# Optimization experiments

Hardware: AMD Instinct MI355X
Metric: run time of the kernel (lower is better)

Reference implementation:

```python
import jax, jax.numpy as jnp
import numpy as np
from jax import lax

ALPHA = 5.0   # ATan surrogate alpha
TAU = 2.0     # LIF tau
HEADS = 16
SCALE = 0.25

@jax.custom_vjp
def atan_spike(x):
    return (x >= 0.0).astype(x.dtype)

def _atan_fwd(x):
    return atan_spike(x), x

def _atan_bwd(x, g):
    # spikingjelly surrogate.ATan: d/dx = alpha/2 / (1 + (pi/2*alpha*x)^2)
    return (g * (ALPHA / 2.0) / (1.0 + (jnp.pi / 2.0 * ALPHA * x) ** 2),)

atan_spike.defvjp(_atan_fwd, _atan_bwd)

def lif(x, v_th=1.0):
    # Multi-step LIF, hard reset to 0, detach_reset=True. x: [T, ...]
    def step(v, xt):
        h = v + (xt - v) / TAU
        s = atan_spike(h - v_th)
        v_new = h * (1.0 - lax.stop_gradient(s))
        return v_new, s
    _, spikes = lax.scan(step, jnp.zeros_like(x[0]), x)
    return spikes

def conv_bn(x, w, gamma, beta, mean, var, eps=1e-5):
    # 1x1 Conv1d (bias=False) + BatchNorm1d (eval stats). x: [..., C, N]
    y = jnp.einsum('oc,...cn->...on', w, x)
    scale = gamma * lax.rsqrt(var + eps)
    return y * scale[:, None] + (beta - mean * scale)[:, None]

def setup_inputs() -> dict:
    key = jax.random.key(0)
    ks = jax.random.split(key, 22)
    T, B, C, H, W = 4, 8, 256, 32, 16
    d = {}
    d['x'] = jax.random.normal(ks[0], (T, B, C, H, W), jnp.float32)
    i = 1
    for n in ['q', 'k', 'v', 'proj']:
        d[n + '_w'] = jax.random.normal(ks[i], (C, C), jnp.float32) / 16.0; i += 1
        d[n + '_gamma'] = jax.random.uniform(ks[i], (C,), jnp.float32, 0.5, 1.5); i += 1
        d[n + '_beta'] = jax.random.normal(ks[i], (C,), jnp.float32) * 0.1; i += 1
        d[n + '_mean'] = jax.random.normal(ks[i], (C,), jnp.float32) * 0.1; i += 1
        d[n + '_var'] = jax.random.uniform(ks[i], (C,), jnp.float32, 0.5, 1.5); i += 1
    return d

def reference(x, q_w, q_gamma, q_beta, q_mean, q_var,
              k_w, k_gamma, k_beta, k_mean, k_var,
              v_w, v_gamma, v_beta, v_mean, v_var,
              proj_w, proj_gamma, proj_beta, proj_mean, proj_var):
    T, B, C, H, W = x.shape
    N = H * W
    hd = C // HEADS
    xf = x.reshape(T, B, C, N)

    def branch(w, g, b, m, v):
        s = lif(conv_bn(xf, w, g, b, m, v))  # [T,B,C,N] binary spikes
        # -> [T,B,heads,N,head_dim]
        return s.transpose(0, 1, 3, 2).reshape(T, B, N, HEADS, hd).transpose(0, 1, 3, 2, 4)

    q = branch(q_w, q_gamma, q_beta, q_mean, q_var)
    k = branch(k_w, k_gamma, k_beta, k_mean, k_var)
    v = branch(v_w, v_gamma, v_beta, v_mean, v_var)

    attn = jnp.einsum('tbhnd,tbhmd->tbhnm', q, k)           # binary q@k^T
    y = jnp.einsum('tbhnm,tbhmd->tbhnd', attn, v) * SCALE   # (attn @ v) * 0.25
    y = y.transpose(0, 1, 2, 4, 3).reshape(T, B, C, N)       # transpose(3,4) then merge heads

    # attn_lif is applied on flatten(0,1): time dim = T*B (faithful to source)
    s = lif(y.reshape(T * B, C, N), v_th=0.5)
    p = conv_bn(s, proj_w, proj_gamma, proj_beta, proj_mean, proj_var)
    out = lif(p.reshape(T, B, C, W, H))  # note W,H swap, as in source
    return out
```

## Files before the change

### kernel.cpp

```cpp
#include <hip/hip_runtime.h>

#define TT 4
#define BB 8
#define CC 256
#define NN 512
#define HEADS 16
#define HD 16

#define GLL16(gp, lp) \
    __builtin_amdgcn_global_load_lds( \
        (const __attribute__((address_space(1))) void*)(gp), \
        (__attribute__((address_space(3))) void*)(lp), 16, 0, 0)

struct WPtrs  { const float* w[4]; };
struct BnPtrs { const float* g[4]; const float* b[4]; const float* m[4]; const float* v[4]; };

__global__ __launch_bounds__(256)
void prep_bn(BnPtrs p, float* __restrict__ sc, float* __restrict__ bi)
{
    int m = blockIdx.x, c = threadIdx.x;
    float rs = __fdiv_rn(1.0f, __fsqrt_rn(__fadd_rn(p.v[m][c], 1e-5f)));
    float s  = __fmul_rn(p.g[m][c], rs);
    sc[m * CC + c] = s;
    bi[m * CC + c] = __fsub_rn(p.b[m][c], __fmul_rn(p.m[m][c], s));
}

__global__ __launch_bounds__(256)
void transpose_w(WPtrs p, float* __restrict__ wt)
{
    __shared__ float t[16][17];
    const int m  = blockIdx.z;
    const float* w = p.w[m];
    const int o0 = blockIdx.y * 16, k0 = blockIdx.x * 16;
    const int tx = threadIdx.x, ty = threadIdx.y;
    t[ty][tx] = w[(size_t)(o0 + ty) * CC + k0 + tx];
    __syncthreads();
    wt[(size_t)m * CC * CC + (size_t)(k0 + ty) * CC + o0 + tx] = t[tx][ty];
}

__global__ __launch_bounds__(256)
void qkv_conv_bn_lif_pack(const float* __restrict__ x,
                          const float* __restrict__ wt,
                          const float* __restrict__ scA,
                          const float* __restrict__ biA,
                          unsigned long long* __restrict__ bits)
{
    __shared__ float Wl[2][32][128];
    __shared__ float Xl[2][32][128];
    __shared__ unsigned char Spk[128][16];

    const int tid = threadIdx.x;
    const int tx = tid & 15;
    const int ty = tid >> 4;
    const int br = blockIdx.z >> 3;
    const int b  = blockIdx.z & 7;
    const int o0 = blockIdx.y * 128;
    const int n0 = blockIdx.x * 128;

    const float* wb = wt + (size_t)br * CC * CC;
    unsigned long long* bout = bits + (size_t)br * (TT * BB * CC * 8);

    float sc[8], bi[8];
#pragma unroll
    for (int i = 0; i < 8; ++i) {
        sc[i] = scA[br * CC + o0 + ty * 8 + i];
        bi[i] = biA[br * CC + o0 + ty * 8 + i];
    }

    auto stage = [&](int s, int buf) {
        const int t  = s >> 3;
        const int k0 = (s & 7) * 32;
        const float* xb = x + (size_t)(t * BB + b) * (CC * NN);
#pragma unroll
        for (int i = 0; i < 4; ++i) {
            int idx = tid + 256 * i;
            int row = idx >> 5, cg = idx & 31;
            GLL16(&wb[(size_t)(k0 + row) * CC + o0 + cg * 4], &Wl[buf][row][cg * 4]);
        }
#pragma unroll
        for (int i = 0; i < 4; ++i) {
            int idx = tid + 256 * i;
            int row = idx >> 5, cg = idx & 31;
            GLL16(&xb[(size_t)(k0 + row) * NN + n0 + cg * 4], &Xl[buf][row][cg * 4]);
        }
    };

    float acc[8][8], vst[8][8];
#pragma unroll
    for (int i = 0; i < 8; ++i)
#pragma unroll
        for (int j = 0; j < 8; ++j) { acc[i][j] = 0.0f; vst[i][j] = 0.0f; }

    stage(0, 0);
    __syncthreads();

    int cur = 0;
    for (int s = 0; s < 32; ++s) {
        if (s < 31) stage(s + 1, cur ^ 1);

#pragma unroll 8
        for (int kk = 0; kk < 32; ++kk) {
            const float4 w0 = *reinterpret_cast<const float4*>(&Wl[cur][kk][ty * 8]);
            const float4 w1 = *reinterpret_cast<const float4*>(&Wl[cur][kk][ty * 8 + 4]);
            const float4 x0 = *reinterpret_cast<const float4*>(&Xl[cur][kk][tx * 8]);
            const float4 x1 = *reinterpret_cast<const float4*>(&Xl[cur][kk][tx * 8 + 4]);
            const float wa[8] = {w0.x, w0.y, w0.z, w0.w, w1.x, w1.y, w1.z, w1.w};
            const float xa[8] = {x0.x, x0.y, x0.z, x0.w, x1.x, x1.y, x1.z, x1.w};
#pragma unroll
            for (int i = 0; i < 8; ++i)
#pragma unroll
                for (int j = 0; j < 8; ++j)
                    acc[i][j] = __fmaf_rn(wa[i], xa[j], acc[i][j]);
        }

        if ((s & 7) == 7) {
            const int t = s >> 3;
#pragma unroll
            for (int i = 0; i < 8; ++i) {
                unsigned int byte = 0u;
#pragma unroll
                for (int j = 0; j < 8; ++j) {
                    float ybn = __fadd_rn(__fmul_rn(acc[i][j], sc[i]), bi[i]);
                    float h   = __fadd_rn(vst[i][j],
                                          __fmul_rn(__fsub_rn(ybn, vst[i][j]), 0.5f));
                    bool sp = (h >= 1.0f);
                    vst[i][j] = sp ? 0.0f : h;
                    byte |= (sp ? 1u : 0u) << j;
                    acc[i][j] = 0.0f;
                }
                Spk[ty * 8 + i][tx] = (unsigned char)byte;
            }
            __syncthreads();
            {
                int o = tid >> 1, ch = tid & 1;
                unsigned long long m =
                    *reinterpret_cast<const unsigned long long*>(&Spk[o][ch * 8]);
                bout[((size_t)(t * BB + b) * CC + o0 + o) * 8 + (blockIdx.x * 2 + ch)] = m;
            }
        }

        __syncthreads();
        cur ^= 1;
    }
}

__global__ __launch_bounds__(256)
void attn_kernel(const unsigned long long* __restrict__ bq,
                 const unsigned long long* __restrict__ bk,
                 const unsigned long long* __restrict__ bv,
                 float* __restrict__ y)
{
    const int blk = blockIdx.x;
    const int h  = blk & 15;
    const int tb = blk >> 4;
    const int tid = threadIdx.x;

    __shared__ unsigned long long kb[16][8], vb[16][8], qb[16][8];
    __shared__ float M[16][16];

    size_t base = ((size_t)tb * CC + h * HD) * 8;
    if (tid < 128) {
        int j = tid >> 3, ch = tid & 7;
        kb[j][ch] = bk[base + j * 8 + ch];
        vb[j][ch] = bv[base + j * 8 + ch];
        qb[j][ch] = bq[base + j * 8 + ch];
    }
    __syncthreads();

    {
        int j = tid >> 4, d = tid & 15;
        int cnt = 0;
#pragma unroll
        for (int ch = 0; ch < 8; ++ch)
            cnt += __popcll(kb[j][ch] & vb[d][ch]);
        M[j][d] = (float)cnt;
    }
    __syncthreads();

    size_t ybase = ((size_t)tb * CC + h * HD) * (size_t)NN;
#pragma unroll
    for (int r = 0; r < 2; ++r) {
        int n = tid + 256 * r;
        int ch = n >> 6, sh = n & 63;
        float acc[16];
#pragma unroll
        for (int d = 0; d < 16; ++d) acc[d] = 0.0f;
#pragma unroll
        for (int j = 0; j < 16; ++j) {
            float bit = (float)((qb[j][ch] >> sh) & 1ULL);
#pragma unroll
            for (int d = 0; d < 16; ++d)
                acc[d] = __fmaf_rn(bit, M[j][d], acc[d]);
        }
#pragma unroll
        for (int d = 0; d < 16; ++d)
            y[ybase + (size_t)d * NN + n] = __fmul_rn(acc[d], 0.25f);
    }
}

__global__ __launch_bounds__(256)
void attn_lif(float* __restrict__ y)
{
    const int e = blockIdx.x * 256 + threadIdx.x;
    float xs[32];
#pragma unroll
    for (int tb = 0; tb < 32; ++tb)
        xs[tb] = y[(size_t)tb * (CC * NN) + e];
    float v = 0.0f;
#pragma unroll
    for (int tb = 0; tb < 32; ++tb) {
        float h = __fadd_rn(v, __fmul_rn(__fsub_rn(xs[tb], v), 0.5f));
        bool sp = (h >= 0.5f);
        y[(size_t)tb * (CC * NN) + e] = sp ? 1.0f : 0.0f;
        v = sp ? 0.0f : h;
    }
}

__global__ __launch_bounds__(256)
void proj_gemm_bn(const float* __restrict__ X,
                  const float* __restrict__ wtp,
                  const float* __restrict__ scP,
                  const float* __restrict__ biP,
                  float* __restrict__ Y)
{
    __shared__ float Wl[2][32][128];
    __shared__ float Xl[2][32][128];

    const int tid = threadIdx.x;
    const int tx = tid & 15;
    const int ty = tid >> 4;
    const int tb = blockIdx.z;
    const int o0 = blockIdx.y * 128;
    const int n0 = blockIdx.x * 128;

    const float* xb = X + (size_t)tb * (CC * NN);

    float sc[8], bi[8];
#pragma unroll
    for (int i = 0; i < 8; ++i) {
        sc[i] = scP[o0 + ty * 8 + i];
        bi[i] = biP[o0 + ty * 8 + i];
    }

    auto stage = [&](int s, int buf) {
        const int k0 = s * 32;
#pragma unroll
        for (int i = 0; i < 4; ++i) {
            int idx = tid + 256 * i;
            int row = idx >> 5, cg = idx & 31;
            GLL16(&wtp[(size_t)(k0 + row) * CC + o0 + cg * 4], &Wl[buf][row][cg * 4]);
        }
#pragma unroll
        for (int i = 0; i < 4; ++i) {
            int idx = tid + 256 * i;
            int row = idx >> 5, cg = idx & 31;
            GLL16(&xb[(size_t)(k0 + row) * NN + n0 + cg * 4], &Xl[buf][row][cg * 4]);
        }
    };

    float acc[8][8];
#pragma unroll
    for (int i = 0; i < 8; ++i)
#pragma unroll
        for (int j = 0; j < 8; ++j) acc[i][j] = 0.0f;

    stage(0, 0);
    __syncthreads();

    int cur = 0;
    for (int s = 0; s < 8; ++s) {
        if (s < 7) stage(s + 1, cur ^ 1);

#pragma unroll 8
        for (int kk = 0; kk < 32; ++kk) {
            const float4 w0 = *reinterpret_cast<const float4*>(&Wl[cur][kk][ty * 8]);
            const float4 w1 = *reinterpret_cast<const float4*>(&Wl[cur][kk][ty * 8 + 4]);
            const float4 x0 = *reinterpret_cast<const float4*>(&Xl[cur][kk][tx * 8]);
            const float4 x1 = *reinterpret_cast<const float4*>(&Xl[cur][kk][tx * 8 + 4]);
            const float wa[8] = {w0.x, w0.y, w0.z, w0.w, w1.x, w1.y, w1.z, w1.w};
            const float xa[8] = {x0.x, x0.y, x0.z, x0.w, x1.x, x1.y, x1.z, x1.w};
#pragma unroll
            for (int i = 0; i < 8; ++i)
#pragma unroll
                for (int j = 0; j < 8; ++j)
                    acc[i][j] = __fmaf_rn(wa[i], xa[j], acc[i][j]);
        }

        __syncthreads();
        cur ^= 1;
    }

    float* Yp = Y + (size_t)tb * (CC * NN);
#pragma unroll
    for (int i = 0; i < 8; ++i) {
        float r[8];
#pragma unroll
        for (int j = 0; j < 8; ++j)
            r[j] = __fadd_rn(__fmul_rn(acc[i][j], sc[i]), bi[i]);
        float4 r0 = make_float4(r[0], r[1], r[2], r[3]);
        float4 r1 = make_float4(r[4], r[5], r[6], r[7]);
        float* dst = &Yp[(size_t)(o0 + ty * 8 + i) * NN + n0 + tx * 8];
        *reinterpret_cast<float4*>(dst) = r0;
        *reinterpret_cast<float4*>(dst + 4) = r1;
    }
}

__global__ __launch_bounds__(256)
void final_lif(const float* __restrict__ Yp, float* __restrict__ out)
{
    const size_t stride = (size_t)BB * CC * NN;
    const int i4 = blockIdx.x * 256 + threadIdx.x;
    float4 v = make_float4(0.f, 0.f, 0.f, 0.f);
#pragma unroll
    for (int t = 0; t < 4; ++t) {
        float4 xv = *reinterpret_cast<const float4*>(&Yp[t * stride + (size_t)i4 * 4]);
        float4 o4;
        float h;
        h = __fadd_rn(v.x, __fmul_rn(__fsub_rn(xv.x, v.x), 0.5f));
        o4.x = (h >= 1.0f) ? 1.0f : 0.0f; v.x = (h >= 1.0f) ? 0.0f : h;
        h = __fadd_rn(v.y, __fmul_rn(__fsub_rn(xv.y, v.y), 0.5f));
        o4.y = (h >= 1.0f) ? 1.0f : 0.0f; v.y = (h >= 1.0f) ? 0.0f : h;
        h = __fadd_rn(v.z, __fmul_rn(__fsub_rn(xv.z, v.z), 0.5f));
        o4.z = (h >= 1.0f) ? 1.0f : 0.0f; v.z = (h >= 1.0f) ? 0.0f : h;
        h = __fadd_rn(v.w, __fmul_rn(__fsub_rn(xv.w, v.w), 0.5f));
        o4.w = (h >= 1.0f) ? 1.0f : 0.0f; v.w = (h >= 1.0f) ? 0.0f : h;
        *reinterpret_cast<float4*>(&out[t * stride + (size_t)i4 * 4]) = o4;
    }
}

extern "C" void kernel_launch(void* const* d_in, const int* in_sizes, int n_in,
                              void* d_out, int out_size, void* d_ws, size_t ws_size,
                              hipStream_t stream) {
    const float* x = (const float*)d_in[0];

    WPtrs wp;
    BnPtrs bp;
    for (int m = 0; m < 4; ++m) {
        wp.w[m] = (const float*)d_in[1 + m * 5 + 0];
        bp.g[m] = (const float*)d_in[1 + m * 5 + 1];
        bp.b[m] = (const float*)d_in[1 + m * 5 + 2];
        bp.m[m] = (const float*)d_in[1 + m * 5 + 3];
        bp.v[m] = (const float*)d_in[1 + m * 5 + 4];
    }

    char* ws = (char*)d_ws;
    float* wt   = (float*)ws;
    float* scA  = (float*)(ws + (1u << 20));
    float* biA  = (float*)(ws + (1u << 20) + 4096);
    unsigned long long* bits = (unsigned long long*)(ws + (1u << 20) + 8192);
    float* ybuf  = (float*)(ws + (1u << 20) + 8192 + 1572864);
    float* ybn_p = (float*)(ws + (1u << 20) + 8192 + 1572864 + 16777216);

    prep_bn<<<4, 256, 0, stream>>>(bp, scA, biA);
    transpose_w<<<dim3(16, 16, 4), dim3(16, 16), 0, stream>>>(wp, wt);

    qkv_conv_bn_lif_pack<<<dim3(4, 2, 24), 256, 0, stream>>>(x, wt, scA, biA, bits);

    const unsigned long long* bq = bits;
    const unsigned long long* bk = bits + 65536;
    const unsigned long long* bv = bits + 131072;
    attn_kernel<<<512, 256, 0, stream>>>(bq, bk, bv, ybuf);
    attn_lif<<<512, 256, 0, stream>>>(ybuf);

    proj_gemm_bn<<<dim3(4, 2, 32), 256, 0, stream>>>(
        ybuf, wt + 3 * CC * CC, scA + 3 * CC, biA + 3 * CC, ybn_p);
    final_lif<<<1024, 256, 0, stream>>>(ybn_p, (float*)d_out);
}
```

Before: 297.3 us.

## Split QKV GEMM from LIF to widen grid, halve proj GEMM tile width

The fused QKV kernel, which looped over time inside each block and so launched only 192 blocks, becomes a plain GEMM+BN over all T*B slices (768 blocks). Its output goes to a float buffer, and a separate LIF kernel then packs spikes with wave ballots. The GEMM thread mapping changes to a 2x2 wave layout, and the projection GEMM tile narrows to 128x64 to double its block count. The aim is more parallelism and occupancy on the GPU, paid for with a 48MB float intermediate written and read back plus an extra launch.

```diff
diff --git a/kernel.cpp b/kernel.cpp
--- a/kernel.cpp
+++ b/kernel.cpp
@@ -39,38 +39,34 @@
 }
 
 __global__ __launch_bounds__(256)
-void qkv_conv_bn_lif_pack(const float* __restrict__ x,
-                          const float* __restrict__ wt,
-                          const float* __restrict__ scA,
-                          const float* __restrict__ biA,
-                          unsigned long long* __restrict__ bits)
+void qkv_gemm_bn(const float* __restrict__ x,
+                 const float* __restrict__ wt,
+                 const float* __restrict__ scA,
+                 const float* __restrict__ biA,
+                 float* __restrict__ ybn3)
 {
     __shared__ float Wl[2][32][128];
     __shared__ float Xl[2][32][128];
-    __shared__ unsigned char Spk[128][16];
-
-    const int tid = threadIdx.x;
-    const int tx = tid & 15;
-    const int ty = tid >> 4;
-    const int br = blockIdx.z >> 3;
-    const int b  = blockIdx.z & 7;
+
+    const int tid  = threadIdx.x;
+    const int wave = tid >> 6;
+    const int lane = tid & 63;
+    const int wr = wave >> 1;
+    const int wc = wave & 1;
+    const int ty = lane >> 3;
+    const int tx = lane & 7;
+    const int br = blockIdx.z >> 5;
+    const int tb = blockIdx.z & 31;
     const int o0 = blockIdx.y * 128;
     const int n0 = blockIdx.x * 128;
+    const int oo = o0 + wr * 64 + ty * 8;
+    const int nn = n0 + wc * 64 + tx * 8;
 
     const float* wb = wt + (size_t)br * CC * CC;
-    unsigned long long* bout = bits + (size_t)br * (TT * BB * CC * 8);
-
-    float sc[8], bi[8];
-#pragma unroll
-    for (int i = 0; i < 8; ++i) {
-        sc[i] = scA[br * CC + o0 + ty * 8 + i];
-        bi[i] = biA[br * CC + o0 + ty * 8 + i];
-    }
+    const float* xb = x + (size_t)tb * (CC * NN);
 
     auto stage = [&](int s, int buf) {
-        const int t  = s >> 3;
-        const int k0 = (s & 7) * 32;
-        const float* xb = x + (size_t)(t * BB + b) * (CC * NN);
+        const int k0 = s * 32;
 #pragma unroll
         for (int i = 0; i < 4; ++i) {
             int idx = tid + 256 * i;
@@ -85,25 +81,25 @@
         }
     };
 
-    float acc[8][8], vst[8][8];
+    float acc[8][8];
 #pragma unroll
     for (int i = 0; i < 8; ++i)
 #pragma unroll
-        for (int j = 0; j < 8; ++j) { acc[i][j] = 0.0f; vst[i][j] = 0.0f; }
+        for (int j = 0; j < 8; ++j) acc[i][j] = 0.0f;
 
     stage(0, 0);
     __syncthreads();
 
     int cur = 0;
-    for (int s = 0; s < 32; ++s) {
-        if (s < 31) stage(s + 1, cur ^ 1);
+    for (int s = 0; s < 8; ++s) {
+        if (s < 7) stage(s + 1, cur ^ 1);
 
 #pragma unroll 8
         for (int kk = 0; kk < 32; ++kk) {
-            const float4 w0 = *reinterpret_cast<const float4*>(&Wl[cur][kk][ty * 8]);
-            const float4 w1 = *reinterpret_cast<const float4*>(&Wl[cur][kk][ty * 8 + 4]);
-            const float4 x0 = *reinterpret_cast<const float4*>(&Xl[cur][kk][tx * 8]);
-            const float4 x1 = *reinterpret_cast<const float4*>(&Xl[cur][kk][tx * 8 + 4]);
+            const float4 w0 = *reinterpret_cast<const float4*>(&Wl[cur][kk][wr * 64 + ty * 8]);
+            const float4 w1 = *reinterpret_cast<const float4*>(&Wl[cur][kk][wr * 64 + ty * 8 + 4]);
+            const float4 x0 = *reinterpret_cast<const float4*>(&Xl[cur][kk][wc * 64 + tx * 8]);
+            const float4 x1 = *reinterpret_cast<const float4*>(&Xl[cur][kk][wc * 64 + tx * 8 + 4]);
             const float wa[8] = {w0.x, w0.y, w0.z, w0.w, w1.x, w1.y, w1.z, w1.w};
             const float xa[8] = {x0.x, x0.y, x0.z, x0.w, x1.x, x1.y, x1.z, x1.w};
 #pragma unroll
@@ -113,34 +109,49 @@
                     acc[i][j] = __fmaf_rn(wa[i], xa[j], acc[i][j]);
         }
 
-        if ((s & 7) == 7) {
-            const int t = s >> 3;
-#pragma unroll
-            for (int i = 0; i < 8; ++i) {
-                unsigned int byte = 0u;
-#pragma unroll
-                for (int j = 0; j < 8; ++j) {
-                    float ybn = __fadd_rn(__fmul_rn(acc[i][j], sc[i]), bi[i]);
-                    float h   = __fadd_rn(vst[i][j],
-                                          __fmul_rn(__fsub_rn(ybn, vst[i][j]), 0.5f));
-                    bool sp = (h >= 1.0f);
-                    vst[i][j] = sp ? 0.0f : h;
-                    byte |= (sp ? 1u : 0u) << j;
-                    acc[i][j] = 0.0f;
-                }
-                Spk[ty * 8 + i][tx] = (unsigned char)byte;
-            }
-            __syncthreads();
-            {
-                int o = tid >> 1, ch = tid & 1;
-                unsigned long long m =
-                    *reinterpret_cast<const unsigned long long*>(&Spk[o][ch * 8]);
-                bout[((size_t)(t * BB + b) * CC + o0 + o) * 8 + (blockIdx.x * 2 + ch)] = m;
-            }
-        }
-
         __syncthreads();
         cur ^= 1;
+    }
+
+    float* Yp = ybn3 + ((size_t)br * 32 + tb) * (CC * NN);
+#pragma unroll
+    for (int i = 0; i < 8; ++i) {
+        const float sc = scA[br * CC + oo + i];
+        const float bi = biA[br * CC + oo + i];
+        float r[8];
+#pragma unroll
+        for (int j = 0; j < 8; ++j)
+            r[j] = __fadd_rn(__fmul_rn(acc[i][j], sc), bi);
+        float* dst = &Yp[(size_t)(oo + i) * NN + nn];
+        *reinterpret_cast<float4*>(dst)     = make_float4(r[0], r[1], r[2], r[3]);
+        *reinterpret_cast<float4*>(dst + 4) = make_float4(r[4], r[5], r[6], r[7]);
+    }
+}
+
+__global__ __launch_bounds__(256)
+void qkv_lif_pack(const float* __restrict__ ybn3,
+                  unsigned long long* __restrict__ bits)
+{
+    const int g = blockIdx.x * 256 + threadIdx.x;
+    const int n = g & 511;
+    const int c = (g >> 9) & 255;
+    const int b = (g >> 17) & 7;
+    const int br = g >> 20;
+
+    const float* src = ybn3 + (size_t)br * 32 * (CC * NN);
+    unsigned long long* bout = bits + (size_t)br * (32 * CC * 8);
+
+    float v = 0.0f;
+#pragma unroll
+    for (int t = 0; t < 4; ++t) {
+        const int tb = t * 8 + b;
+        float xv = src[((size_t)tb * CC + c) * NN + n];
+        float h  = __fadd_rn(v, __fmul_rn(__fsub_rn(xv, v), 0.5f));
+        bool sp = (h >= 1.0f);
+        v = sp ? 0.0f : h;
+        unsigned long long msk = __ballot(sp ? 1 : 0);
+        if ((threadIdx.x & 63) == 0)
+            bout[((size_t)tb * CC + c) * 8 + (n >> 6)] = msk;
     }
 }
 
@@ -224,23 +235,16 @@
                   float* __restrict__ Y)
 {
     __shared__ float Wl[2][32][128];
-    __shared__ float Xl[2][32][128];
+    __shared__ float Xl[2][32][64];
 
     const int tid = threadIdx.x;
     const int tx = tid & 15;
     const int ty = tid >> 4;
     const int tb = blockIdx.z;
     const int o0 = blockIdx.y * 128;
-    const int n0 = blockIdx.x * 128;
+    const int n0 = blockIdx.x * 64;
 
     const float* xb = X + (size_t)tb * (CC * NN);
-
-    float sc[8], bi[8];
-#pragma unroll
-    for (int i = 0; i < 8; ++i) {
-        sc[i] = scP[o0 + ty * 8 + i];
-        bi[i] = biP[o0 + ty * 8 + i];
-    }
 
     auto stage = [&](int s, int buf) {
         const int k0 = s * 32;
@@ -251,18 +255,18 @@
             GLL16(&wtp[(size_t)(k0 + row) * CC + o0 + cg * 4], &Wl[buf][row][cg * 4]);
         }
 #pragma unroll
-        for (int i = 0; i < 4; ++i) {
+        for (int i = 0; i < 2; ++i) {
             int idx = tid + 256 * i;
-            int row = idx >> 5, cg = idx & 31;
+            int row = idx >> 4, cg = idx & 15;
             GLL16(&xb[(size_t)(k0 + row) * NN + n0 + cg * 4], &Xl[buf][row][cg * 4]);
         }
     };
 
-    float acc[8][8];
+    float acc[8][4];
 #pragma unroll
     for (int i = 0; i < 8; ++i)
 #pragma unroll
-        for (int j = 0; j < 8; ++j) acc[i][j] = 0.0f;
+        for (int j = 0; j < 4; ++j) acc[i][j] = 0.0f;
 
     stage(0, 0);
     __syncthreads();
@@ -275,14 +279,13 @@
         for (int kk = 0; kk < 32; ++kk) {
             const float4 w0 = *reinterpret_cast<const float4*>(&Wl[cur][kk][ty * 8]);
             const float4 w1 = *reinterpret_cast<const float4*>(&Wl[cur][kk][ty * 8 + 4]);
-            const float4 x0 = *reinterpret_cast<const float4*>(&Xl[cur][kk][tx * 8]);
-            const float4 x1 = *reinterpret_cast<const float4*>(&Xl[cur][kk][tx * 8 + 4]);
+            const float4 xv = *reinterpret_cast<const float4*>(&Xl[cur][kk][tx * 4]);
             const float wa[8] = {w0.x, w0.y, w0.z, w0.w, w1.x, w1.y, w1.z, w1.w};
-            const float xa[8] = {x0.x, x0.y, x0.z, x0.w, x1.x, x1.y, x1.z, x1.w};
+            const float xa[4] = {xv.x, xv.y, xv.z, xv.w};
 #pragma unroll
             for (int i = 0; i < 8; ++i)
 #pragma unroll
-                for (int j = 0; j < 8; ++j)
+                for (int j = 0; j < 4; ++j)
                     acc[i][j] = __fmaf_rn(wa[i], xa[j], acc[i][j]);
         }
 
@@ -293,15 +296,14 @@
     float* Yp = Y + (size_t)tb * (CC * NN);
 #pragma unroll
     for (int i = 0; i < 8; ++i) {
-        float r[8];
-#pragma unroll
-        for (int j = 0; j < 8; ++j)
-            r[j] = __fadd_rn(__fmul_rn(acc[i][j], sc[i]), bi[i]);
-        float4 r0 = make_float4(r[0], r[1], r[2], r[3]);
-        float4 r1 = make_float4(r[4], r[5], r[6], r[7]);
-        float* dst = &Yp[(size_t)(o0 + ty * 8 + i) * NN + n0 + tx * 8];
-        *reinterpret_cast<float4*>(dst) = r0;
-        *reinterpret_cast<float4*>(dst + 4) = r1;
+        const float sc = scP[o0 + ty * 8 + i];
+        const float bi = biP[o0 + ty * 8 + i];
+        float r[4];
+#pragma unroll
+        for (int j = 0; j < 4; ++j)
+            r[j] = __fadd_rn(__fmul_rn(acc[i][j], sc), bi);
+        *reinterpret_cast<float4*>(&Yp[(size_t)(o0 + ty * 8 + i) * NN + n0 + tx * 4])
+            = make_float4(r[0], r[1], r[2], r[3]);
     }
 }
 
@@ -348,13 +350,16 @@
     float* scA  = (float*)(ws + (1u << 20));
     float* biA  = (float*)(ws + (1u << 20) + 4096);
     unsigned long long* bits = (unsigned long long*)(ws + (1u << 20) + 8192);
-    float* ybuf  = (float*)(ws + (1u << 20) + 8192 + 1572864);
-    float* ybn_p = (float*)(ws + (1u << 20) + 8192 + 1572864 + 16777216);
+    char*  big  = ws + (1u << 20) + 8192 + 1572864;
+    float* ybn3 = (float*)big;
+    float* ybuf = (float*)big;
+    float* ybn_p = (float*)(big + (16u << 20));
 
     prep_bn<<<4, 256, 0, stream>>>(bp, scA, biA);
     transpose_w<<<dim3(16, 16, 4), dim3(16, 16), 0, stream>>>(wp, wt);
 
-    qkv_conv_bn_lif_pack<<<dim3(4, 2, 24), 256, 0, stream>>>(x, wt, scA, biA, bits);
+    qkv_gemm_bn<<<dim3(4, 2, 96), 256, 0, stream>>>(x, wt, scA, biA, ybn3);
+    qkv_lif_pack<<<12288, 256, 0, stream>>>(ybn3, bits);
 
     const unsigned long long* bq = bits;
     const unsigned long long* bk = bits + 65536;
@@ -362,7 +367,7 @@
     attn_kernel<<<512, 256, 0, stream>>>(bq, bk, bv, ybuf);
     attn_lif<<<512, 256, 0, stream>>>(ybuf);
 
-    proj_gemm_bn<<<dim3(4, 2, 32), 256, 0, stream>>>(
+    proj_gemm_bn<<<dim3(8, 2, 32), 256, 0, stream>>>(
         ybuf, wt + 3 * CC * CC, scA + 3 * CC, biA + 3 * CC, ybn_p);
     final_lif<<<1024, 256, 0, stream>>>(ybn_p, (float*)d_out);
 }
```

Result: faster. 251.5 us (-15.4%).
